# Optimization experiments

Measured on AMD Instinct MI355X. Metric: run time of the kernel, lower is better.

The kernel has to match this reference:

```python
import jax, jax.numpy as jnp
import numpy as np

D_MODEL = 1024
N_HEADS = 16
D_HEAD = D_MODEL // N_HEADS
GN_EPS = 1e-5


def setup_inputs() -> dict:
    key = jax.random.key(0)
    ks = jax.random.split(key, 5)
    B, T = 2, 2048
    s = 1.0 / np.sqrt(D_MODEL)
    x = jax.random.normal(ks[0], (B, T, D_MODEL), dtype=jnp.float32)
    W_q = jax.random.normal(ks[1], (D_MODEL, D_MODEL), dtype=jnp.float32) * s
    W_k = jax.random.normal(ks[2], (D_MODEL, D_MODEL), dtype=jnp.float32) * s
    W_v = jax.random.normal(ks[3], (D_MODEL, D_MODEL), dtype=jnp.float32) * s
    W_o = jax.random.normal(ks[4], (D_MODEL, D_MODEL), dtype=jnp.float32) * s
    gn_weight = jnp.ones((D_MODEL,), dtype=jnp.float32)
    gn_bias = jnp.zeros((D_MODEL,), dtype=jnp.float32)
    return {"x": x, "W_q": W_q, "W_k": W_k, "W_v": W_v, "W_o": W_o,
            "gn_weight": gn_weight, "gn_bias": gn_bias}


def reference(x, W_q, W_k, W_v, W_o, gn_weight, gn_bias):
    B, T, _ = x.shape
    H, Dh = N_HEADS, D_HEAD
    # Projections (nn.Linear: y = x @ W.T), split heads -> [B, T, H, Dh]
    q = (x @ W_q.T).reshape(B, T, H, Dh)
    k = (x @ W_k.T).reshape(B, T, H, Dh)
    v = (x @ W_v.T).reshape(B, T, H, Dh)

    # Per-head causal decay mask D_h[i, j] = gamma_h^(i-j) for i >= j else 0
    gammas = jnp.asarray([1.0 - 2.0 ** (-5.0 - i) for i in range(H)],
                         dtype=jnp.float32)  # [H]
    idx = jnp.arange(T, dtype=jnp.float32)
    diff = idx[:, None] - idx[None, :]  # [T, T]
    decay = jnp.where(diff >= 0,
                      gammas[:, None, None] ** jnp.maximum(diff, 0.0),
                      0.0)  # [H, T, T]

    scale = jnp.sqrt(jnp.asarray(Dh, dtype=x.dtype))
    qk = jnp.einsum('bthd,bshd->bhts', q, k)          # [B, H, T, T]
    attn = qk * decay[None] / scale
    y = jnp.einsum('bhts,bshd->bthd', attn, v)        # [B, T, H, Dh]

    # GroupNorm(n_heads groups) over channels-last-transposed layout:
    # torch applies it to [B, d_model, T]; each group = one head's Dh channels,
    # normalized over (Dh, T).
    yg = y.transpose(0, 2, 3, 1)                      # [B, H, Dh, T]
    mean = yg.mean(axis=(2, 3), keepdims=True)
    var = yg.var(axis=(2, 3), keepdims=True)
    yn = (yg - mean) / jnp.sqrt(var + GN_EPS)
    yn = yn * gn_weight.reshape(1, H, Dh, 1) + gn_bias.reshape(1, H, Dh, 1)
    y = yn.transpose(0, 3, 1, 2).reshape(B, T, H * Dh)  # [B, T, d_model]
    return y @ W_o.T
```

## Files before the change

### kernel.cpp

```cpp
#include <hip/hip_runtime.h>
#include <math.h>

#define TSEQ 2048
#define NB   2
#define DM   1024
#define NH   16
#define DH   64
#define GN_EPS 1e-5f

typedef short v8s __attribute__((ext_vector_type(8)));
typedef short v4s __attribute__((ext_vector_type(4)));
typedef float v4f __attribute__((ext_vector_type(4)));

__device__ __forceinline__ short f2bf(float f) {
    union { float f; unsigned u; } c; c.f = f;
    unsigned u = c.u;
    unsigned r = (u + 0x7fffu + ((u >> 16) & 1u)) >> 16;
    return (short)r;
}
__device__ __forceinline__ float bf2f(short s) {
    union { unsigned u; float f; } c; c.u = ((unsigned)(unsigned short)s) << 16;
    return c.f;
}

__device__ __forceinline__ unsigned cvtpk_bf16(float lo, float hi) {
    unsigned r;
    asm("v_cvt_pk_bf16_f32 %0, %1, %2" : "=v"(r) : "v"(lo), "v"(hi));
    return r;
}

__device__ __forceinline__ void gl_lds16(const void* g, void* l) {
    __builtin_amdgcn_global_load_lds(
        (const __attribute__((address_space(1))) void*)g,
        (__attribute__((address_space(3))) void*)l, 16, 0, 0);
}

__global__ __launch_bounds__(256) void cast_kernel(
    const float* __restrict__ x,
    const float* __restrict__ Wq, const float* __restrict__ Wk,
    const float* __restrict__ Wv, const float* __restrict__ Wo,
    short* __restrict__ xbf, short* __restrict__ wbf)
{
    const int NX = NB * TSEQ * DM;
    const int NW = DM * DM;
    const int total4 = (NX + 4 * NW) / 4;
    for (int i = blockIdx.x * 256 + threadIdx.x; i < total4;
         i += gridDim.x * 256) {
        int e = i * 4;
        const float* src; short* dst;
        if (e < NX) { src = x + e; dst = xbf + e; }
        else {
            int o = e - NX;
            int w = o >> 20;
            int r = o & (NW - 1);
            src = (w == 0 ? Wq : w == 1 ? Wk : w == 2 ? Wv : Wo) + r;
            dst = wbf + o;
        }
        v4f v = *(const v4f*)src;
        v4s s;
        #pragma unroll
        for (int j = 0; j < 4; ++j) s[j] = f2bf(v[j]);
        *(v4s*)dst = s;
    }
}

template <bool SWAP>
__device__ __forceinline__ void mm_loop_db(
    const char* Agp, const char* Bgp, char* lds,
    int t, int lr, int g, int wr, int wc, v4f acc[4][4])
{
    int soff[4], sdst[4];
    #pragma unroll
    for (int p = 0; p < 4; ++p) {
        int i = p * 256 + t;
        int row = i >> 3;
        int cp  = (i & 7) * 16;
        soff[p] = row * (DM * 2) + (cp ^ ((row & 7) << 4));
        sdst[p] = (p * 256 + (t & 192)) * 16;
    }
    const int swz = (lr & 7) << 4;

    #pragma unroll
    for (int p = 0; p < 4; ++p) {
        gl_lds16(Agp + (size_t)soff[p], lds + sdst[p]);
        gl_lds16(Bgp + (size_t)soff[p], lds + 16384 + sdst[p]);
    }

    for (int kt = 0; kt < DM / 64; ++kt) {
        const char* cur = lds + (kt & 1) * 32768;
        asm volatile("s_waitcnt vmcnt(0)" ::: "memory");
        __syncthreads();

        if (kt < DM / 64 - 1) {
            char* nxt = lds + ((kt + 1) & 1) * 32768;
            const int kb = (kt + 1) * 128;
            #pragma unroll
            for (int p = 0; p < 4; ++p) {
                gl_lds16(Agp + (size_t)soff[p] + kb, nxt + sdst[p]);
                gl_lds16(Bgp + (size_t)soff[p] + kb, nxt + 16384 + sdst[p]);
            }
        }

        v8s bfr[4][2];
        #pragma unroll
        for (int j = 0; j < 4; ++j) {
            int rowb = wc + j * 16 + lr;
            #pragma unroll
            for (int ks = 0; ks < 2; ++ks)
                bfr[j][ks] = *(const v8s*)(cur + 16384 + rowb * 128
                               + ((ks * 64 + g * 16) ^ swz));
        }
        #pragma unroll
        for (int i = 0; i < 4; ++i) {
            int rowa = wr + i * 16 + lr;
            v8s a0 = *(const v8s*)(cur + rowa * 128 + ((g * 16) ^ swz));
            v8s a1 = *(const v8s*)(cur + rowa * 128 + ((64 + g * 16) ^ swz));
            #pragma unroll
            for (int j = 0; j < 4; ++j) {
                if (SWAP) {
                    acc[i][j] = __builtin_amdgcn_mfma_f32_16x16x32_bf16(
                        bfr[j][0], a0, acc[i][j], 0, 0, 0);
                    acc[i][j] = __builtin_amdgcn_mfma_f32_16x16x32_bf16(
                        bfr[j][1], a1, acc[i][j], 0, 0, 0);
                } else {
                    acc[i][j] = __builtin_amdgcn_mfma_f32_16x16x32_bf16(
                        a0, bfr[j][0], acc[i][j], 0, 0, 0);
                    acc[i][j] = __builtin_amdgcn_mfma_f32_16x16x32_bf16(
                        a1, bfr[j][1], acc[i][j], 0, 0, 0);
                }
            }
        }
    }
}

__global__ __launch_bounds__(256, 2) void gemm_qkv_mfma(
    const short* __restrict__ xbf, const short* __restrict__ wbf,
    short* __restrict__ Qb, short* __restrict__ Kb,
    short* __restrict__ Kt, short* __restrict__ Vt)
{
    const int bid = blockIdx.x;
    const int swizb = (bid & 7) * 96 + (bid >> 3);
    const int z = swizb >> 8;
    const int rem = swizb & 255;
    const int n0 = (rem & 7) * 128, m0 = (rem >> 3) * 128;

    const int t = threadIdx.x, l = t & 63, w = t >> 6;
    const int wr = (w >> 1) * 64, wc = (w & 1) * 64;
    const int lr = l & 15, g = l >> 4, lg4 = g * 4;

    __shared__ char lds[65536];

    v4f acc[4][4];
    #pragma unroll
    for (int i = 0; i < 4; ++i)
        #pragma unroll
        for (int j = 0; j < 4; ++j) acc[i][j] = (v4f){0.f, 0.f, 0.f, 0.f};

    const char* Agp = (const char*)(xbf + (size_t)m0 * DM);
    const char* Bgp = (const char*)(wbf + (size_t)z * (DM * DM) + (size_t)n0 * DM);

    if (z == 0) {
        mm_loop_db<true>(Agp, Bgp, lds, t, lr, g, wr, wc, acc);
        const int head = (n0 + wc) >> 6;
        const float l2g = log2f(1.0f - exp2f(-5.0f - (float)head));
        float fac[4];
        #pragma unroll
        for (int i = 0; i < 4; ++i) {
            int tl = (m0 + wr + i * 16 + lr) & 63;
            fac[i] = exp2f(fmaf(l2g, (float)tl, -3.0f));
        }
        #pragma unroll
        for (int i = 0; i < 4; ++i) {
            int mrow = m0 + wr + i * 16 + lr;
            #pragma unroll
            for (int j = 0; j < 4; ++j) {
                int ncol = n0 + wc + j * 16 + lg4;
                v4s pk;
                #pragma unroll
                for (int r = 0; r < 4; ++r) pk[r] = f2bf(acc[i][j][r] * fac[i]);
                *(v4s*)(Qb + (size_t)mrow * DM + ncol) = pk;
            }
        }
    } else if (z == 1) {
        mm_loop_db<false>(Agp, Bgp, lds, t, lr, g, wr, wc, acc);
        float l2gj[4];
        #pragma unroll
        for (int j = 0; j < 4; ++j) {
            int hh = (n0 + wc + j * 16 + lr) >> 6;
            l2gj[j] = -log2f(1.0f - exp2f(-5.0f - (float)hh));
        }
        #pragma unroll
        for (int i = 0; i < 4; ++i) {
            int row  = m0 + wr + i * 16 + lg4;
            int bidx = row >> 11, tb = row & (TSEQ - 1);
            #pragma unroll
            for (int j = 0; j < 4; ++j) {
                int col = n0 + wc + j * 16 + lr;
                v4s pk;
                #pragma unroll
                for (int r = 0; r < 4; ++r) {
                    int tl = (row + r) & 63;
                    float fc = exp2f(l2gj[j] * (float)tl);
                    short bv = f2bf(acc[i][j][r] * fc);
                    Kb[(size_t)(row + r) * DM + col] = bv;
                    pk[r] = bv;
                }
                *(v4s*)(Kt + ((size_t)bidx << 21) + ((size_t)col << 11) + tb) = pk;
            }
        }
    } else {
        mm_loop_db<false>(Agp, Bgp, lds, t, lr, g, wr, wc, acc);
        #pragma unroll
        for (int i = 0; i < 4; ++i) {
            int row  = m0 + wr + i * 16 + lg4;
            int bidx = row >> 11, tb = row & (TSEQ - 1);
            #pragma unroll
            for (int j = 0; j < 4; ++j) {
                int col = n0 + wc + j * 16 + lr;
                v4s pk;
                #pragma unroll
                for (int r = 0; r < 4; ++r) pk[r] = f2bf(acc[i][j][r]);
                *(v4s*)(Vt + ((size_t)bidx << 21) + ((size_t)col << 11) + tb) = pk;
            }
        }
    }
}

__global__ __launch_bounds__(256, 2) void chunk_kv(
    const short* __restrict__ Kt, const short* __restrict__ Vt,
    short* __restrict__ At)
{
    const int bid = blockIdx.x;
    const int c = bid & 31, bh = bid >> 5;
    const int b = bh >> 4, h = bh & 15;
    const int tid = threadIdx.x, l = tid & 63, w = tid >> 6;
    const int lr = l & 15, g = l >> 4;

    const size_t rowbase = ((size_t)b * DM + h * 64);

    v8s kf[2], vf[4][2];
    {
        const short* kp = Kt + (rowbase + 16 * w + lr) * TSEQ + 64 * c;
        kf[0] = *(const v8s*)(kp + g * 8);
        kf[1] = *(const v8s*)(kp + 32 + g * 8);
    }
    #pragma unroll
    for (int j = 0; j < 4; ++j) {
        const short* vp = Vt + (rowbase + j * 16 + lr) * TSEQ + 64 * c;
        vf[j][0] = *(const v8s*)(vp + g * 8);
        vf[j][1] = *(const v8s*)(vp + 32 + g * 8);
    }

    v4f acc[4];
    #pragma unroll
    for (int j = 0; j < 4; ++j) acc[j] = (v4f){0.f, 0.f, 0.f, 0.f};

    #pragma unroll
    for (int j = 0; j < 4; ++j) {
        acc[j] = __builtin_amdgcn_mfma_f32_16x16x32_bf16(kf[0], vf[j][0], acc[j], 0, 0, 0);
        acc[j] = __builtin_amdgcn_mfma_f32_16x16x32_bf16(kf[1], vf[j][1], acc[j], 0, 0, 0);
    }

    short* Ab = At + (((size_t)bh * 32 + c) << 12);
    #pragma unroll
    for (int j = 0; j < 4; ++j) {
        v4s pk;
        #pragma unroll
        for (int r = 0; r < 4; ++r) pk[r] = f2bf(acc[j][r]);
        *(v4s*)(Ab + (j * 16 + lr) * 64 + 16 * w + g * 4) = pk;
    }
}

__global__ __launch_bounds__(256) void chunk_scan(
    const short* __restrict__ At, short* __restrict__ St)
{
    const int idx = blockIdx.x * 256 + threadIdx.x;
    const int bh = idx >> 12;
    const int h  = bh & 15;
    const float l2g = log2f(1.0f - exp2f(-5.0f - (float)h));
    const float g64 = exp2f(l2g * 64.0f);

    const size_t base = ((size_t)bh << 17) + (idx & 4095);
    float state = 0.0f;
    #pragma unroll
    for (int c = 1; c < 32; ++c) {
        float a = bf2f(At[base + ((size_t)(c - 1) << 12)]);
        state = g64 * (state + a);
        St[base + ((size_t)c << 12)] = f2bf(state);
    }
}

__global__ __launch_bounds__(256, 2) void chunk_out(
    const short* __restrict__ Qb, const short* __restrict__ Kb,
    const short* __restrict__ Vt, const short* __restrict__ St,
    short* __restrict__ Ybf, float* __restrict__ psums)
{
    const int bid = blockIdx.x;
    const int xcd = bid & 7, r8 = bid >> 3;
    const int bh  = xcd * 4 + (r8 >> 5);
    const int c   = r8 & 31;
    const int b = bh >> 4, h = bh & 15;
    const int tid = threadIdx.x, l = tid & 63, w = tid >> 6;
    const int lr = l & 15, g = l >> 4;

    __shared__ short strip[64 * 64];
    __shared__ float tr[64][68];
    __shared__ float red[8];

    const size_t rowQK = ((size_t)(b * TSEQ + 64 * c)) * DM + h * 64;

    v8s qf[4][2];
    #pragma unroll
    for (int j = 0; j < 4; ++j) {
        const short* qp = Qb + rowQK + (size_t)(j * 16 + lr) * DM;
        qf[j][0] = *(const v8s*)(qp + g * 8);
        qf[j][1] = *(const v8s*)(qp + 32 + g * 8);
    }
    v8s kf0, kf1;
    {
        const short* kp = Kb + rowQK + (size_t)(16 * w + lr) * DM;
        kf0 = *(const v8s*)(kp + g * 8);
        kf1 = *(const v8s*)(kp + 32 + g * 8);
    }
    v8s sf0 = {}, sf1 = {};
    if (c > 0) {
        const short* sp = St + (((size_t)bh * 32 + c) << 12) + (16 * w + lr) * 64;
        sf0 = *(const v8s*)(sp + g * 8);
        sf1 = *(const v8s*)(sp + 32 + g * 8);
    }
    v8s vf0, vf1;
    {
        const short* vp = Vt + ((size_t)(b * DM + h * 64) + 16 * w + lr) * TSEQ
                          + 64 * c;
        vf0 = *(const v8s*)(vp + g * 8);
        vf1 = *(const v8s*)(vp + 32 + g * 8);
    }

    v4f s[4];
    #pragma unroll
    for (int j = 0; j < 4; ++j) {
        v4f a = (v4f){0.f, 0.f, 0.f, 0.f};
        a = __builtin_amdgcn_mfma_f32_16x16x32_bf16(kf0, qf[j][0], a, 0, 0, 0);
        a = __builtin_amdgcn_mfma_f32_16x16x32_bf16(kf1, qf[j][1], a, 0, 0, 0);
        s[j] = a;
    }

    v4f y[4];
    #pragma unroll
    for (int j = 0; j < 4; ++j) y[j] = (v4f){0.f, 0.f, 0.f, 0.f};
    if (c > 0) {
        #pragma unroll
        for (int j = 0; j < 4; ++j) {
            y[j] = __builtin_amdgcn_mfma_f32_16x16x32_bf16(sf0, qf[j][0], y[j], 0, 0, 0);
            y[j] = __builtin_amdgcn_mfma_f32_16x16x32_bf16(sf1, qf[j][1], y[j], 0, 0, 0);
        }
    }

    #pragma unroll
    for (int j = 0; j < 4; ++j) {
        v4f vv = s[j];
        #pragma unroll
        for (int r = 0; r < 4; ++r)
            if ((j * 16 + lr) - (16 * w + g * 4 + r) < 0) vv[r] = 0.0f;
        unsigned u0 = cvtpk_bf16(vv[0], vv[1]);
        unsigned u1 = cvtpk_bf16(vv[2], vv[3]);
        int byte = ((j * 16 + lr) * 128 + 32 * w + g * 8) ^ ((lr & 7) << 4);
        *(unsigned long long*)((char*)strip + byte) =
            (unsigned long long)u0 | ((unsigned long long)u1 << 32);
    }
    __syncthreads();

    #pragma unroll
    for (int j = 0; j < 4; ++j) {
        int rb = (j * 16 + lr) * 128;
        int sw = (lr & 7) << 4;
        v8s sB0 = *(const v8s*)((char*)strip + ((rb + g * 16) ^ sw));
        v8s sB1 = *(const v8s*)((char*)strip + ((rb + 64 + g * 16) ^ sw));
        y[j] = __builtin_amdgcn_mfma_f32_16x16x32_bf16(vf0, sB0, y[j], 0, 0, 0);
        y[j] = __builtin_amdgcn_mfma_f32_16x16x32_bf16(vf1, sB1, y[j], 0, 0, 0);
    }

    float lsum = 0.f, lsq = 0.f;
    #pragma unroll
    for (int j = 0; j < 4; ++j)
        #pragma unroll
        for (int r = 0; r < 4; ++r) {
            float vy = y[j][r];
            lsum += vy; lsq += vy * vy;
        }
    #pragma unroll
    for (int m = 32; m; m >>= 1) {
        lsum += __shfl_xor(lsum, m, 64);
        lsq  += __shfl_xor(lsq,  m, 64);
    }
    if (l == 0) { red[w] = lsum; red[4 + w] = lsq; }

    #pragma unroll
    for (int j = 0; j < 4; ++j)
        #pragma unroll
        for (int r = 0; r < 4; ++r)
            tr[j * 16 + lr][16 * w + g * 4 + r] = y[j][r];
    __syncthreads();

    if (tid == 0) {
        float* ps = psums + ((size_t)bh * 32 + c) * 2;
        ps[0] = red[0] + red[1] + red[2] + red[3];
        ps[1] = red[4] + red[5] + red[6] + red[7];
    }

    #pragma unroll
    for (int u = 0; u < 4; ++u) {
        int row  = (tid >> 4) + u * 16;
        int col4 = (tid & 15) * 4;
        v4f val = *(const v4f*)&tr[row][col4];
        v4s pk;
        #pragma unroll
        for (int r = 0; r < 4; ++r) pk[r] = f2bf(val[r]);
        *(v4s*)&Ybf[(size_t)(b * TSEQ + 64 * c + row) * DM + h * 64 + col4] = pk;
    }
}

__global__ __launch_bounds__(256) void gn_finalize(
    const float* __restrict__ psums,
    const float* __restrict__ gnw, const float* __restrict__ gnb,
    float* __restrict__ scale, float* __restrict__ shift)
{
    int idx = blockIdx.x * 256 + threadIdx.x;
    if (idx >= NB * DM) return;
    int bb = idx >> 10;
    int ch = idx & (DM - 1);
    int hh = ch >> 6;
    int bh = bb * 16 + hh;

    float s = 0.f, q = 0.f;
    #pragma unroll
    for (int k = 0; k < 32; ++k) {
        s += psums[((size_t)bh * 32 + k) * 2];
        q += psums[((size_t)bh * 32 + k) * 2 + 1];
    }
    const float n = (float)(DH * TSEQ);
    float mean = s / n;
    float var  = q / n - mean * mean;
    float rstd = rsqrtf(var + GN_EPS);
    float sc = rstd * gnw[ch];
    scale[idx] = sc;
    shift[idx] = gnb[ch] - mean * sc;
}

__global__ __launch_bounds__(256) void wo_prep(
    const short* __restrict__ Wob, const float* __restrict__ scale,
    const float* __restrict__ shift,
    short* __restrict__ Wo2, float* __restrict__ bias)
{
    const int tid = threadIdx.x, l = tid & 63, w = tid >> 6;
    const int bn = blockIdx.x * 4 + w;
    const int b = bn >> 10, n = bn & 1023;
    const int k0 = l * 16;

    const short* wp = Wob + (size_t)n * DM + k0;
    v8s w0 = *(const v8s*)wp;
    v8s w1 = *(const v8s*)(wp + 8);
    const float* sc = scale + b * DM + k0;
    const float* sh = shift + b * DM + k0;

    v8s o0, o1;
    float bsum = 0.f;
    #pragma unroll
    for (int j = 0; j < 8; ++j) {
        float wf = bf2f(w0[j]);
        o0[j] = f2bf(wf * sc[j]);
        bsum = fmaf(sh[j], wf, bsum);
    }
    #pragma unroll
    for (int j = 0; j < 8; ++j) {
        float wf = bf2f(w1[j]);
        o1[j] = f2bf(wf * sc[8 + j]);
        bsum = fmaf(sh[8 + j], wf, bsum);
    }
    short* op = Wo2 + ((size_t)b * DM + n) * DM + k0;
    *(v8s*)op = o0;
    *(v8s*)(op + 8) = o1;

    #pragma unroll
    for (int m = 32; m; m >>= 1) bsum += __shfl_xor(bsum, m, 64);
    if (l == 0) bias[bn] = bsum;
}

__global__ __launch_bounds__(256, 2) void gemm_out_mfma(
    const short* __restrict__ Ybf, const short* __restrict__ Wo2,
    const float* __restrict__ bias, float* __restrict__ out)
{
    const int bid = blockIdx.x;
    const int swizb = (bid & 7) * 32 + (bid >> 3);
    const int n0 = (swizb & 7) * 128, m0 = (swizb >> 3) * 128;
    const int b = m0 >> 11;
    const int t = threadIdx.x, l = t & 63, w = t >> 6;
    const int wr = (w >> 1) * 64, wc = (w & 1) * 64;
    const int lr = l & 15, g = l >> 4;

    __shared__ char lds[65536];

    v4f acc[4][4];
    #pragma unroll
    for (int i = 0; i < 4; ++i)
        #pragma unroll
        for (int j = 0; j < 4; ++j) acc[i][j] = (v4f){0.f, 0.f, 0.f, 0.f};

    const char* Agp = (const char*)(Ybf + (size_t)m0 * DM);
    const char* Bgp = (const char*)(Wo2 + (size_t)b * DM * DM + (size_t)n0 * DM);

    mm_loop_db<true>(Agp, Bgp, lds, t, lr, g, wr, wc, acc);

    #pragma unroll
    for (int i = 0; i < 4; ++i) {
        int mrow = m0 + wr + i * 16 + lr;
        #pragma unroll
        for (int j = 0; j < 4; ++j) {
            int ncol = n0 + wc + j * 16 + g * 4;
            v4f bv = *(const v4f*)&bias[b * DM + ncol];
            v4f o = acc[i][j] + bv;
            *(v4f*)&out[(size_t)mrow * DM + ncol] = o;
        }
    }
}

extern "C" void kernel_launch(void* const* d_in, const int* in_sizes, int n_in,
                              void* d_out, int out_size, void* d_ws, size_t ws_size,
                              hipStream_t stream)
{
    const float* x   = (const float*)d_in[0];
    const float* Wq  = (const float*)d_in[1];
    const float* Wk  = (const float*)d_in[2];
    const float* Wv  = (const float*)d_in[3];
    const float* Wo  = (const float*)d_in[4];
    const float* gnw = (const float*)d_in[5];
    const float* gnb = (const float*)d_in[6];
    float* out = (float*)d_out;

    char* wsb = (char*)d_ws;
    size_t o = 0;
    short* Qb   = (short*)(wsb + o); o += (size_t)NB * TSEQ * DM * 2;
    short* Kb   = (short*)(wsb + o); o += (size_t)NB * TSEQ * DM * 2;
    short* Kt   = (short*)(wsb + o); o += (size_t)NB * TSEQ * DM * 2;
    short* Vt   = (short*)(wsb + o); o += (size_t)NB * TSEQ * DM * 2;
    short* xbf  = (short*)(wsb + o); o += (size_t)NB * TSEQ * DM * 2;
    short* wbf  = (short*)(wsb + o); o += (size_t)4 * DM * DM * 2;
    short* Ybf  = (short*)(wsb + o); o += (size_t)NB * TSEQ * DM * 2;
    short* St   = (short*)(wsb + o); o += (size_t)NB * TSEQ * DM * 2;
    short* Wo2  = (short*)(wsb + o); o += (size_t)NB * DM * DM * 2;
    float* psums = (float*)(wsb + o); o += (size_t)32 * 32 * 2 * 4;
    float* scale = (float*)(wsb + o); o += (size_t)NB * DM * 4;
    float* shift = (float*)(wsb + o); o += (size_t)NB * DM * 4;
    float* bias  = (float*)(wsb + o); o += (size_t)NB * DM * 4;
    if (ws_size < o) return;

    short* At = xbf;

    cast_kernel<<<2048, 256, 0, stream>>>(x, Wq, Wk, Wv, Wo, xbf, wbf);
    gemm_qkv_mfma<<<dim3(768), 256, 0, stream>>>(xbf, wbf, Qb, Kb, Kt, Vt);
    chunk_kv<<<dim3(1024), 256, 0, stream>>>(Kt, Vt, At);
    chunk_scan<<<dim3(512), 256, 0, stream>>>(At, St);
    chunk_out<<<dim3(1024), 256, 0, stream>>>(Qb, Kb, Vt, St, Ybf, psums);
    gn_finalize<<<dim3((NB * DM + 255) / 256), 256, 0, stream>>>(
        psums, gnw, gnb, scale, shift);
    wo_prep<<<dim3(512), 256, 0, stream>>>(
        wbf + 3 * (size_t)DM * DM, scale, shift, Wo2, bias);
    gemm_out_mfma<<<dim3(256), 256, 0, stream>>>(Ybf, Wo2, bias, out);
}
```

Baseline: 89.78 us.

## Use single-buffered LDS in QKV GEMM to raise occupancy

Replaces the double-buffered 64KB LDS main loop in the QKV projection GEMM with a single-buffered 32KB version that loads, waits, computes and syncs on each k-step. Launch bounds go from 2 to 3 blocks per CU. The goal is to hide memory latency by running more resident workgroups instead of through in-block prefetch. In exchange, the load/compute overlap inside each block is lost and every k-step now has two barriers.

```diff
diff --git a/kernel.cpp b/kernel.cpp
--- a/kernel.cpp
+++ b/kernel.cpp
@@ -65,8 +65,8 @@
 }
 
 template <bool SWAP>
-__device__ __forceinline__ void mm_loop_db(
-    const char* Agp, const char* Bgp, char* lds,
+__device__ __forceinline__ void mm_loop(
+    const char* Agp, const char* Bgp, short* Asm, short* Bsm,
     int t, int lr, int g, int wr, int wc, v4f acc[4][4])
 {
     int soff[4], sdst[4];
@@ -80,6 +80,65 @@
     }
     const int swz = (lr & 7) << 4;
 
+    for (int kt = 0; kt < DM / 64; ++kt) {
+        const int kb = kt * 128;
+        #pragma unroll
+        for (int p = 0; p < 4; ++p) {
+            gl_lds16(Agp + (size_t)soff[p] + kb, (char*)Asm + sdst[p]);
+            gl_lds16(Bgp + (size_t)soff[p] + kb, (char*)Bsm + sdst[p]);
+        }
+        asm volatile("s_waitcnt vmcnt(0)" ::: "memory");
+        __syncthreads();
+
+        v8s bfr[4][2];
+        #pragma unroll
+        for (int j = 0; j < 4; ++j) {
+            int rowb = wc + j * 16 + lr;
+            #pragma unroll
+            for (int ks = 0; ks < 2; ++ks)
+                bfr[j][ks] = *(const v8s*)((const char*)Bsm + rowb * 128
+                               + ((ks * 64 + g * 16) ^ swz));
+        }
+        #pragma unroll
+        for (int i = 0; i < 4; ++i) {
+            int rowa = wr + i * 16 + lr;
+            v8s a0 = *(const v8s*)((const char*)Asm + rowa * 128 + ((g * 16) ^ swz));
+            v8s a1 = *(const v8s*)((const char*)Asm + rowa * 128 + ((64 + g * 16) ^ swz));
+            #pragma unroll
+            for (int j = 0; j < 4; ++j) {
+                if (SWAP) {
+                    acc[i][j] = __builtin_amdgcn_mfma_f32_16x16x32_bf16(
+                        bfr[j][0], a0, acc[i][j], 0, 0, 0);
+                    acc[i][j] = __builtin_amdgcn_mfma_f32_16x16x32_bf16(
+                        bfr[j][1], a1, acc[i][j], 0, 0, 0);
+                } else {
+                    acc[i][j] = __builtin_amdgcn_mfma_f32_16x16x32_bf16(
+                        a0, bfr[j][0], acc[i][j], 0, 0, 0);
+                    acc[i][j] = __builtin_amdgcn_mfma_f32_16x16x32_bf16(
+                        a1, bfr[j][1], acc[i][j], 0, 0, 0);
+                }
+            }
+        }
+        __syncthreads();
+    }
+}
+
+template <bool SWAP>
+__device__ __forceinline__ void mm_loop_db(
+    const char* Agp, const char* Bgp, char* lds,
+    int t, int lr, int g, int wr, int wc, v4f acc[4][4])
+{
+    int soff[4], sdst[4];
+    #pragma unroll
+    for (int p = 0; p < 4; ++p) {
+        int i = p * 256 + t;
+        int row = i >> 3;
+        int cp  = (i & 7) * 16;
+        soff[p] = row * (DM * 2) + (cp ^ ((row & 7) << 4));
+        sdst[p] = (p * 256 + (t & 192)) * 16;
+    }
+    const int swz = (lr & 7) << 4;
+
     #pragma unroll
     for (int p = 0; p < 4; ++p) {
         gl_lds16(Agp + (size_t)soff[p], lds + sdst[p]);
@@ -133,7 +192,7 @@
     }
 }
 
-__global__ __launch_bounds__(256, 2) void gemm_qkv_mfma(
+__global__ __launch_bounds__(256, 3) void gemm_qkv_mfma(
     const short* __restrict__ xbf, const short* __restrict__ wbf,
     short* __restrict__ Qb, short* __restrict__ Kb,
     short* __restrict__ Kt, short* __restrict__ Vt)
@@ -148,7 +207,8 @@
     const int wr = (w >> 1) * 64, wc = (w & 1) * 64;
     const int lr = l & 15, g = l >> 4, lg4 = g * 4;
 
-    __shared__ char lds[65536];
+    __shared__ short As[128 * 64];
+    __shared__ short Bs[128 * 64];
 
     v4f acc[4][4];
     #pragma unroll
@@ -160,7 +220,7 @@
     const char* Bgp = (const char*)(wbf + (size_t)z * (DM * DM) + (size_t)n0 * DM);
 
     if (z == 0) {
-        mm_loop_db<true>(Agp, Bgp, lds, t, lr, g, wr, wc, acc);
+        mm_loop<true>(Agp, Bgp, As, Bs, t, lr, g, wr, wc, acc);
         const int head = (n0 + wc) >> 6;
         const float l2g = log2f(1.0f - exp2f(-5.0f - (float)head));
         float fac[4];
@@ -182,7 +242,7 @@
             }
         }
     } else if (z == 1) {
-        mm_loop_db<false>(Agp, Bgp, lds, t, lr, g, wr, wc, acc);
+        mm_loop<false>(Agp, Bgp, As, Bs, t, lr, g, wr, wc, acc);
         float l2gj[4];
         #pragma unroll
         for (int j = 0; j < 4; ++j) {
@@ -209,7 +269,7 @@
             }
         }
     } else {
-        mm_loop_db<false>(Agp, Bgp, lds, t, lr, g, wr, wc, acc);
+        mm_loop<false>(Agp, Bgp, As, Bs, t, lr, g, wr, wc, acc);
         #pragma unroll
         for (int i = 0; i < 4; ++i) {
             int row  = m0 + wr + i * 16 + lg4;
```

Result: no change. 88.57 us, median of 2 (-1.3%).

## Fuse Q/K/V projections into one GEMM kernel sharing the x tile

Applied to the files above, without the earlier changes.

Replaces the three separate Q, K and V GEMM tile groups (768 blocks of 128x128) with one fused kernel of 512 blocks. Each block loads a 128x64 x tile once and multiplies it against 64-column slices of all three weight matrices, cutting redundant reads of x. Each block now covers a single head, so the decay factor is computed once per block. The new main loop is single-buffered with a full vmcnt(0) wait and a barrier every k-step, dropping the double buffering of the old loop, and three accumulator sets raise register pressure.

```diff
diff --git a/kernel.cpp b/kernel.cpp
--- a/kernel.cpp
+++ b/kernel.cpp
@@ -64,6 +64,162 @@
     }
 }
 
+__global__ __launch_bounds__(256, 2) void gemm_qkv_fused(
+    const short* __restrict__ xbf, const short* __restrict__ wbf,
+    short* __restrict__ Qb, short* __restrict__ Kb,
+    short* __restrict__ Kt, short* __restrict__ Vt)
+{
+    const int bid = blockIdx.x;
+    const int xcd = bid & 7, ch = bid >> 3;
+    const int sm = xcd >> 1, sn = xcd & 1;
+    const int m0 = (sm * 8 + (ch >> 3)) * 128;
+    const int n0 = (sn * 8 + (ch & 7)) * 64;
+
+    const int t = threadIdx.x, l = t & 63, w = t >> 6;
+    const int wm = (w >> 1) * 64, wn = (w & 1) * 32;
+    const int lr = l & 15, g = l >> 4;
+    const int swz = (lr & 7) << 4;
+
+    __shared__ short As[128 * 64];
+    __shared__ short Bs[3][64 * 64];
+
+    v4f acc[3][4][2];
+    #pragma unroll
+    for (int z = 0; z < 3; ++z)
+        #pragma unroll
+        for (int i = 0; i < 4; ++i)
+            #pragma unroll
+            for (int j = 0; j < 2; ++j) acc[z][i][j] = (v4f){0.f,0.f,0.f,0.f};
+
+    const char* Agp = (const char*)(xbf + (size_t)m0 * DM);
+    const char* Bgp = (const char*)(wbf + (size_t)n0 * DM);
+    const size_t ZS = (size_t)DM * DM * 2;
+
+    int soffA[4], sdstA[4], soffB[2], sdstB[2];
+    #pragma unroll
+    for (int p = 0; p < 4; ++p) {
+        int c = p * 256 + t;
+        int row = c >> 3, u = c & 7;
+        soffA[p] = row * (DM * 2) + ((u * 16) ^ ((row & 7) << 4));
+        sdstA[p] = (p * 256 + (t & 192)) * 16;
+    }
+    #pragma unroll
+    for (int p = 0; p < 2; ++p) {
+        int c = p * 256 + t;
+        int row = c >> 3, u = c & 7;
+        soffB[p] = row * (DM * 2) + ((u * 16) ^ ((row & 7) << 4));
+        sdstB[p] = (p * 256 + (t & 192)) * 16;
+    }
+
+    for (int kt = 0; kt < DM / 64; ++kt) {
+        const int kb = kt * 128;
+        #pragma unroll
+        for (int p = 0; p < 4; ++p)
+            gl_lds16(Agp + (size_t)soffA[p] + kb, (char*)As + sdstA[p]);
+        #pragma unroll
+        for (int z = 0; z < 3; ++z)
+            #pragma unroll
+            for (int p = 0; p < 2; ++p)
+                gl_lds16(Bgp + ZS * z + (size_t)soffB[p] + kb,
+                         (char*)Bs[z] + sdstB[p]);
+        asm volatile("s_waitcnt vmcnt(0)" ::: "memory");
+        __syncthreads();
+
+        v8s af[4][2];
+        #pragma unroll
+        for (int i = 0; i < 4; ++i) {
+            int rowa = wm + i * 16 + lr;
+            af[i][0] = *(const v8s*)((const char*)As + rowa * 128 + ((g * 16) ^ swz));
+            af[i][1] = *(const v8s*)((const char*)As + rowa * 128 + ((64 + g * 16) ^ swz));
+        }
+        #pragma unroll
+        for (int z = 0; z < 3; ++z) {
+            #pragma unroll
+            for (int j = 0; j < 2; ++j) {
+                int rowb = wn + j * 16 + lr;
+                v8s b0 = *(const v8s*)((const char*)Bs[z] + rowb * 128 + ((g * 16) ^ swz));
+                v8s b1 = *(const v8s*)((const char*)Bs[z] + rowb * 128 + ((64 + g * 16) ^ swz));
+                #pragma unroll
+                for (int i = 0; i < 4; ++i) {
+                    if (z == 0) {
+                        acc[0][i][j] = __builtin_amdgcn_mfma_f32_16x16x32_bf16(
+                            b0, af[i][0], acc[0][i][j], 0, 0, 0);
+                        acc[0][i][j] = __builtin_amdgcn_mfma_f32_16x16x32_bf16(
+                            b1, af[i][1], acc[0][i][j], 0, 0, 0);
+                    } else {
+                        acc[z][i][j] = __builtin_amdgcn_mfma_f32_16x16x32_bf16(
+                            af[i][0], b0, acc[z][i][j], 0, 0, 0);
+                        acc[z][i][j] = __builtin_amdgcn_mfma_f32_16x16x32_bf16(
+                            af[i][1], b1, acc[z][i][j], 0, 0, 0);
+                    }
+                }
+            }
+        }
+        __syncthreads();
+    }
+
+    const int head = n0 >> 6;
+    const float l2g = log2f(1.0f - exp2f(-5.0f - (float)head));
+
+    {
+        float fac[4];
+        #pragma unroll
+        for (int i = 0; i < 4; ++i) {
+            int tl = (m0 + wm + i * 16 + lr) & 63;
+            fac[i] = exp2f(fmaf(l2g, (float)tl, -3.0f));
+        }
+        #pragma unroll
+        for (int i = 0; i < 4; ++i) {
+            int mrow = m0 + wm + i * 16 + lr;
+            #pragma unroll
+            for (int j = 0; j < 2; ++j) {
+                int ncol = n0 + wn + j * 16 + g * 4;
+                v4s pk;
+                #pragma unroll
+                for (int r = 0; r < 4; ++r) pk[r] = f2bf(acc[0][i][j][r] * fac[i]);
+                *(v4s*)(Qb + (size_t)mrow * DM + ncol) = pk;
+            }
+        }
+    }
+    {
+        const float l2gk = -l2g;
+        #pragma unroll
+        for (int i = 0; i < 4; ++i) {
+            int row  = m0 + wm + i * 16 + g * 4;
+            int bidx = row >> 11, tb = row & (TSEQ - 1);
+            #pragma unroll
+            for (int j = 0; j < 2; ++j) {
+                int col = n0 + wn + j * 16 + lr;
+                v4s pk;
+                #pragma unroll
+                for (int r = 0; r < 4; ++r) {
+                    int tl = (row + r) & 63;
+                    float fc = exp2f(l2gk * (float)tl);
+                    short bv = f2bf(acc[1][i][j][r] * fc);
+                    Kb[(size_t)(row + r) * DM + col] = bv;
+                    pk[r] = bv;
+                }
+                *(v4s*)(Kt + ((size_t)bidx << 21) + ((size_t)col << 11) + tb) = pk;
+            }
+        }
+    }
+    {
+        #pragma unroll
+        for (int i = 0; i < 4; ++i) {
+            int row  = m0 + wm + i * 16 + g * 4;
+            int bidx = row >> 11, tb = row & (TSEQ - 1);
+            #pragma unroll
+            for (int j = 0; j < 2; ++j) {
+                int col = n0 + wn + j * 16 + lr;
+                v4s pk;
+                #pragma unroll
+                for (int r = 0; r < 4; ++r) pk[r] = f2bf(acc[2][i][j][r]);
+                *(v4s*)(Vt + ((size_t)bidx << 21) + ((size_t)col << 11) + tb) = pk;
+            }
+        }
+    }
+}
+
 template <bool SWAP>
 __device__ __forceinline__ void mm_loop_db(
     const char* Agp, const char* Bgp, char* lds,
@@ -128,99 +284,6 @@
                     acc[i][j] = __builtin_amdgcn_mfma_f32_16x16x32_bf16(
                         a1, bfr[j][1], acc[i][j], 0, 0, 0);
                 }
-            }
-        }
-    }
-}
-
-__global__ __launch_bounds__(256, 2) void gemm_qkv_mfma(
-    const short* __restrict__ xbf, const short* __restrict__ wbf,
-    short* __restrict__ Qb, short* __restrict__ Kb,
-    short* __restrict__ Kt, short* __restrict__ Vt)
-{
-    const int bid = blockIdx.x;
-    const int swizb = (bid & 7) * 96 + (bid >> 3);
-    const int z = swizb >> 8;
-    const int rem = swizb & 255;
-    const int n0 = (rem & 7) * 128, m0 = (rem >> 3) * 128;
-
-    const int t = threadIdx.x, l = t & 63, w = t >> 6;
-    const int wr = (w >> 1) * 64, wc = (w & 1) * 64;
-    const int lr = l & 15, g = l >> 4, lg4 = g * 4;
-
-    __shared__ char lds[65536];
-
-    v4f acc[4][4];
-    #pragma unroll
-    for (int i = 0; i < 4; ++i)
-        #pragma unroll
-        for (int j = 0; j < 4; ++j) acc[i][j] = (v4f){0.f, 0.f, 0.f, 0.f};
-
-    const char* Agp = (const char*)(xbf + (size_t)m0 * DM);
-    const char* Bgp = (const char*)(wbf + (size_t)z * (DM * DM) + (size_t)n0 * DM);
-
-    if (z == 0) {
-        mm_loop_db<true>(Agp, Bgp, lds, t, lr, g, wr, wc, acc);
-        const int head = (n0 + wc) >> 6;
-        const float l2g = log2f(1.0f - exp2f(-5.0f - (float)head));
-        float fac[4];
-        #pragma unroll
-        for (int i = 0; i < 4; ++i) {
-            int tl = (m0 + wr + i * 16 + lr) & 63;
-            fac[i] = exp2f(fmaf(l2g, (float)tl, -3.0f));
-        }
-        #pragma unroll
-        for (int i = 0; i < 4; ++i) {
-            int mrow = m0 + wr + i * 16 + lr;
-            #pragma unroll
-            for (int j = 0; j < 4; ++j) {
-                int ncol = n0 + wc + j * 16 + lg4;
-                v4s pk;
-                #pragma unroll
-                for (int r = 0; r < 4; ++r) pk[r] = f2bf(acc[i][j][r] * fac[i]);
-                *(v4s*)(Qb + (size_t)mrow * DM + ncol) = pk;
-            }
-        }
-    } else if (z == 1) {
-        mm_loop_db<false>(Agp, Bgp, lds, t, lr, g, wr, wc, acc);
-        float l2gj[4];
-        #pragma unroll
-        for (int j = 0; j < 4; ++j) {
-            int hh = (n0 + wc + j * 16 + lr) >> 6;
-            l2gj[j] = -log2f(1.0f - exp2f(-5.0f - (float)hh));
-        }
-        #pragma unroll
-        for (int i = 0; i < 4; ++i) {
-            int row  = m0 + wr + i * 16 + lg4;
-            int bidx = row >> 11, tb = row & (TSEQ - 1);
-            #pragma unroll
-            for (int j = 0; j < 4; ++j) {
-                int col = n0 + wc + j * 16 + lr;
-                v4s pk;
-                #pragma unroll
-                for (int r = 0; r < 4; ++r) {
-                    int tl = (row + r) & 63;
-                    float fc = exp2f(l2gj[j] * (float)tl);
-                    short bv = f2bf(acc[i][j][r] * fc);
-                    Kb[(size_t)(row + r) * DM + col] = bv;
-                    pk[r] = bv;
-                }
-                *(v4s*)(Kt + ((size_t)bidx << 21) + ((size_t)col << 11) + tb) = pk;
-            }
-        }
-    } else {
-        mm_loop_db<false>(Agp, Bgp, lds, t, lr, g, wr, wc, acc);
-        #pragma unroll
-        for (int i = 0; i < 4; ++i) {
-            int row  = m0 + wr + i * 16 + lg4;
-            int bidx = row >> 11, tb = row & (TSEQ - 1);
-            #pragma unroll
-            for (int j = 0; j < 4; ++j) {
-                int col = n0 + wc + j * 16 + lr;
-                v4s pk;
-                #pragma unroll
-                for (int r = 0; r < 4; ++r) pk[r] = f2bf(acc[i][j][r]);
-                *(v4s*)(Vt + ((size_t)bidx << 21) + ((size_t)col << 11) + tb) = pk;
             }
         }
     }
@@ -557,7 +620,7 @@
     short* At = xbf;
 
     cast_kernel<<<2048, 256, 0, stream>>>(x, Wq, Wk, Wv, Wo, xbf, wbf);
-    gemm_qkv_mfma<<<dim3(768), 256, 0, stream>>>(xbf, wbf, Qb, Kb, Kt, Vt);
+    gemm_qkv_fused<<<dim3(512), 256, 0, stream>>>(xbf, wbf, Qb, Kb, Kt, Vt);
     chunk_kv<<<dim3(1024), 256, 0, stream>>>(Kt, Vt, At);
     chunk_scan<<<dim3(512), 256, 0, stream>>>(At, St);
     chunk_out<<<dim3(1024), 256, 0, stream>>>(Qb, Kb, Vt, St, Ybf, psums);
```

Result: no change. 88.17 us (-1.8%).
